# Kernel tuning notes

Measured on AMD Instinct MI355X. Metric: run time of the kernel, lower is better.

The kernel has to match this reference:

```python
import jax, jax.numpy as jnp
import numpy as np

B, L, D = 4096, 200, 64
N_ITEMS, N_USERS, N_RATINGS = 100000, 100000, 5


def setup_inputs() -> dict:
    key = jax.random.key(0)
    ks = jax.random.split(key, 10)
    nodes = jax.random.randint(ks[0], (B,), 0, N_USERS)
    history_uv = jax.random.randint(ks[1], (B, L), 0, N_ITEMS)
    history_r = jax.random.randint(ks[2], (B, L), 0, N_RATINGS)
    s = 1.0 / np.sqrt(D)
    v2e = jax.random.normal(ks[3], (N_ITEMS, D), dtype=jnp.float32)
    r2e = jax.random.normal(ks[4], (N_RATINGS, D), dtype=jnp.float32)
    # torch Linear: weight is [out, in]
    w1_W = jax.random.uniform(ks[5], (D, 2 * D), dtype=jnp.float32, minval=-s, maxval=s)
    w1_b = jax.random.uniform(ks[6], (D,), dtype=jnp.float32, minval=-s, maxval=s)
    w2_W = jax.random.uniform(ks[7], (D, D), dtype=jnp.float32, minval=-s, maxval=s)
    w2_b = jax.random.uniform(ks[8], (D,), dtype=jnp.float32, minval=-s, maxval=s)
    return {
        "v2e": v2e, "r2e": r2e,
        "w1_W": w1_W, "w1_b": w1_b, "w2_W": w2_W, "w2_b": w2_b,
        "nodes": nodes, "history_uv": history_uv, "history_r": history_r,
    }


def reference(v2e, r2e, w1_W, w1_b, w2_W, w2_b, nodes, history_uv, history_r):
    # Gather item and rating embeddings for every (node, history slot): [B, L, D]
    e_uv = v2e[history_uv]
    e_r = r2e[history_r]
    # concat -> [B, L, 2D], two-layer MLP with ReLU
    x = jnp.concatenate([e_uv, e_r], axis=-1)
    h = jax.nn.relu(jnp.einsum("bli,oi->blo", x, w1_W) + w1_b)
    o = jax.nn.relu(jnp.einsum("bli,oi->blo", h, w2_W) + w2_b)
    # uv=True branch: plain mean over the history dimension (nodes/u2e unused)
    return jnp.mean(o, axis=1)  # [B, D]
```

## Files before the change

### kernel.cpp

```cpp
#include <hip/hip_runtime.h>

#define NITEMS 100000
#define NRATE  5
#define BB     4096
#define LL     200
#define DD     64
#define NTILES 6250
#define NWAVES 2048

typedef short short8  __attribute__((ext_vector_type(8)));
typedef float f32x4   __attribute__((ext_vector_type(4)));
typedef float f32x2   __attribute__((ext_vector_type(2)));
typedef int   i32x4   __attribute__((ext_vector_type(4)));
typedef int   i32x2   __attribute__((ext_vector_type(2)));

static __device__ __forceinline__ short f2bf(float f) {
  return (short)((__builtin_bit_cast(unsigned, f) + 0x8000u) >> 16);
}
static __device__ __forceinline__ unsigned pk2bf(float a, float b) {
  const unsigned ua = __builtin_bit_cast(unsigned, a) + 0x8000u;
  const unsigned ub = __builtin_bit_cast(unsigned, b) + 0x8000u;
  return __builtin_amdgcn_perm(ub, ua, 0x07060302u);
}
static __device__ __forceinline__ int kperm(int p) {
  return ((p & 3) << 4) | (p >> 2);
}

__global__ __launch_bounds__(256) void k_pre(
    const float* __restrict__ v2e, const float* __restrict__ r2e,
    const float* __restrict__ w1W, const float* __restrict__ w1b,
    const float* __restrict__ w2W,
    unsigned char* __restrict__ pre8, short* __restrict__ w2p,
    float* __restrict__ r5p)
{
  const int tid = threadIdx.x;
  const int blk = blockIdx.x;

  if (blk >= 512) {
    for (int idx = tid; idx < 64 * 64; idx += 256) {
      const int o = idx >> 6, p = idx & 63;
      w2p[idx] = f2bf(w2W[o * 64 + kperm(p)]);
    }
    for (int idx = tid; idx < NRATE * 64; idx += 256) {
      const int r = idx >> 6, p = idx & 63;
      const int o = kperm(p);
      const float4* wr = reinterpret_cast<const float4*>(w1W + o * 128 + 64);
      const float4* rr = reinterpret_cast<const float4*>(r2e + r * 64);
      float s = w1b[o];
#pragma unroll
      for (int q = 0; q < 16; ++q) {
        const float4 a = wr[q], b = rr[q];
        s += a.x * b.x + a.y * b.y + a.z * b.z + a.w * b.w;
      }
      r5p[r * 64 + p] = s;
    }
    return;
  }

  const int wave = tid >> 6, lane = tid & 63;
  const int n = lane & 15, quad = lane >> 4;
  const int gw = blk * 4 + wave;
  const int ntile = (gw < (NTILES - 3 * NWAVES)) ? 4 : 3;

  const int q0 = ((n >> 1) & 3) * 16 + (n >> 3) * 8 + (n & 1) * 4;

  short8 bfr[2][4];
#pragma unroll
  for (int nt = 0; nt < 4; ++nt)
#pragma unroll
    for (int kh = 0; kh < 2; ++kh) {
      const float4* p = reinterpret_cast<const float4*>(
          w1W + (nt * 16 + n) * 128 + kh * 32 + quad * 8);
      const float4 x0 = p[0], x1 = p[1];
      i32x4 pk = {(int)pk2bf(x0.x, x0.y), (int)pk2bf(x0.z, x0.w),
                  (int)pk2bf(x1.x, x1.y), (int)pk2bf(x1.z, x1.w)};
      bfr[kh][nt] = __builtin_bit_cast(short8, pk);
    }

  int tile = gw;
  float4 cur0, cur1, cur2, cur3;
  {
    const size_t row = (size_t)(tile * 16 + n);
    const float4* p = reinterpret_cast<const float4*>(v2e + row * 64 + quad * 8);
    cur0 = p[0]; cur1 = p[1];
    const float4* q = reinterpret_cast<const float4*>(v2e + row * 64 + 32 + quad * 8);
    cur2 = q[0]; cur3 = q[1];
  }

  for (int it = 0; it < ntile; ++it) {
    const int next = tile + NWAVES;
    float4 nx0, nx1, nx2, nx3;
    if (it + 1 < ntile) {
      const size_t row = (size_t)(next * 16 + n);
      const float4* p = reinterpret_cast<const float4*>(v2e + row * 64 + quad * 8);
      nx0 = p[0]; nx1 = p[1];
      const float4* q = reinterpret_cast<const float4*>(v2e + row * 64 + 32 + quad * 8);
      nx2 = q[0]; nx3 = q[1];
    }

    short8 afr[2];
    {
      i32x4 pk0 = {(int)pk2bf(cur0.x, cur0.y), (int)pk2bf(cur0.z, cur0.w),
                   (int)pk2bf(cur1.x, cur1.y), (int)pk2bf(cur1.z, cur1.w)};
      afr[0] = __builtin_bit_cast(short8, pk0);
      i32x4 pk1 = {(int)pk2bf(cur2.x, cur2.y), (int)pk2bf(cur2.z, cur2.w),
                   (int)pk2bf(cur3.x, cur3.y), (int)pk2bf(cur3.z, cur3.w)};
      afr[1] = __builtin_bit_cast(short8, pk1);
    }

    f32x4 d[4];
#pragma unroll
    for (int nt = 0; nt < 4; ++nt) {
      f32x4 z = {0.f, 0.f, 0.f, 0.f};
      z = __builtin_amdgcn_mfma_f32_16x16x32_bf16(afr[0], bfr[0][nt], z, 0, 0, 0);
      z = __builtin_amdgcn_mfma_f32_16x16x32_bf16(afr[1], bfr[1][nt], z, 0, 0, 0);
      d[nt] = z;
    }

    const int ib = tile * 16;
#pragma unroll
    for (int r = 0; r < 4; ++r) {
      const int item = ib + quad * 4 + r;
      int pkd = 0;
      pkd = __builtin_amdgcn_cvt_pk_fp8_f32(d[0][r], d[1][r], pkd, false);
      pkd = __builtin_amdgcn_cvt_pk_fp8_f32(d[2][r], d[3][r], pkd, true);
      *reinterpret_cast<int*>(pre8 + (size_t)item * 64 + q0) = pkd;
    }

    tile = next;
    cur0 = nx0; cur1 = nx1; cur2 = nx2; cur3 = nx3;
  }
}

__global__ __launch_bounds__(256) void k_main(
    const unsigned char* __restrict__ pre8, const float* __restrict__ r5p,
    const short* __restrict__ w2p, const float* __restrict__ w2b,
    const int* __restrict__ huv, const int* __restrict__ hrr,
    float* __restrict__ out)
{
  __shared__ __align__(16) float s_r5[4][5 * 68];

  const int tid  = threadIdx.x;
  const int wave = tid >> 6, lane = tid & 63;
  const int n = lane & 15, quad = lane >> 4;
  const int b = blockIdx.x * 4 + wave;

#pragma unroll
  for (int i = 0; i < 5; ++i) {
    const int idx = i * 64 + lane;
    s_r5[wave][(idx >> 6) * 68 + (idx & 63)] = r5p[idx];
  }

  const int* hu = huv + b * LL;
  const int* hr = hrr + b * LL;

  int iv[13], ir[13];
#pragma unroll
  for (int t = 0; t < 12; ++t) {
    iv[t] = hu[t * 16 + n];
    ir[t] = hr[t * 16 + n];
  }
  {
    const int lc = min(192 + n, LL - 1);
    iv[12] = hu[lc];
    ir[12] = hr[lc];
  }

  i32x4 g[13];
#pragma unroll
  for (int t = 0; t < 13; ++t)
    g[t] = *reinterpret_cast<const i32x4*>(
        pre8 + (size_t)iv[t] * 64 + quad * 16);

  short8 bfr[2][4];
#pragma unroll
  for (int nt = 0; nt < 4; ++nt)
#pragma unroll
    for (int kh = 0; kh < 2; ++kh)
      bfr[kh][nt] = *reinterpret_cast<const short8*>(
          w2p + (nt * 16 + n) * 64 + kh * 32 + quad * 8);

  f32x4 zb[4];
#pragma unroll
  for (int nt = 0; nt < 4; ++nt) {
    const float bv = w2b[nt * 16 + n];
    zb[nt] = f32x4{bv, bv, bv, bv};
  }

  const float tailm = (quad < 2) ? 1.0f : 0.0f;
  f32x2 acc2[4] = {{0.f, 0.f}, {0.f, 0.f}, {0.f, 0.f}, {0.f, 0.f}};

#pragma unroll
  for (int t = 0; t < 13; ++t) {
    const float* rbase = &s_r5[wave][ir[t] * 68 + quad * 8];
    short8 afr[2];
    {
      const f32x2* rp = reinterpret_cast<const f32x2*>(rbase);
      f32x2 p0 = __builtin_amdgcn_cvt_pk_f32_fp8(g[t][0], false) + rp[0];
      f32x2 p1 = __builtin_amdgcn_cvt_pk_f32_fp8(g[t][0], true)  + rp[1];
      f32x2 p2 = __builtin_amdgcn_cvt_pk_f32_fp8(g[t][1], false) + rp[2];
      f32x2 p3 = __builtin_amdgcn_cvt_pk_f32_fp8(g[t][1], true)  + rp[3];
      i32x4 hpk = {
        (int)pk2bf(fmaxf(p0.x, 0.f), fmaxf(p0.y, 0.f)),
        (int)pk2bf(fmaxf(p1.x, 0.f), fmaxf(p1.y, 0.f)),
        (int)pk2bf(fmaxf(p2.x, 0.f), fmaxf(p2.y, 0.f)),
        (int)pk2bf(fmaxf(p3.x, 0.f), fmaxf(p3.y, 0.f))};
      afr[0] = __builtin_bit_cast(short8, hpk);
    }
    {
      const f32x2* rp = reinterpret_cast<const f32x2*>(rbase + 32);
      f32x2 p0 = __builtin_amdgcn_cvt_pk_f32_fp8(g[t][2], false) + rp[0];
      f32x2 p1 = __builtin_amdgcn_cvt_pk_f32_fp8(g[t][2], true)  + rp[1];
      f32x2 p2 = __builtin_amdgcn_cvt_pk_f32_fp8(g[t][3], false) + rp[2];
      f32x2 p3 = __builtin_amdgcn_cvt_pk_f32_fp8(g[t][3], true)  + rp[3];
      i32x4 hpk = {
        (int)pk2bf(fmaxf(p0.x, 0.f), fmaxf(p0.y, 0.f)),
        (int)pk2bf(fmaxf(p1.x, 0.f), fmaxf(p1.y, 0.f)),
        (int)pk2bf(fmaxf(p2.x, 0.f), fmaxf(p2.y, 0.f)),
        (int)pk2bf(fmaxf(p3.x, 0.f), fmaxf(p3.y, 0.f))};
      afr[1] = __builtin_bit_cast(short8, hpk);
    }

    f32x4 d[4];
#pragma unroll
    for (int nt = 0; nt < 4; ++nt) {
      f32x4 z = zb[nt];
      z = __builtin_amdgcn_mfma_f32_16x16x32_bf16(afr[0], bfr[0][nt], z, 0, 0, 0);
      z = __builtin_amdgcn_mfma_f32_16x16x32_bf16(afr[1], bfr[1][nt], z, 0, 0, 0);
      d[nt] = z;
    }

#pragma unroll
    for (int nt = 0; nt < 4; ++nt) {
      const float m0 = fmaxf(d[nt][0], 0.f), m1 = fmaxf(d[nt][1], 0.f);
      const float m2 = fmaxf(d[nt][2], 0.f), m3 = fmaxf(d[nt][3], 0.f);
      f32x2 s = {m0 + m1, m2 + m3};
      if (t == 12) { s.x *= tailm; s.y *= tailm; }
      acc2[nt] += s;
    }
  }

  float acc[4];
#pragma unroll
  for (int nt = 0; nt < 4; ++nt) {
    float v = acc2[nt].x + acc2[nt].y;
    v += __shfl_xor(v, 16, 64);
    v += __shfl_xor(v, 32, 64);
    acc[nt] = v;
  }

  out[b * 64 + quad * 16 + n] = acc[quad] * (1.0f / (float)LL);
}

__global__ __launch_bounds__(256) void k_fallback(
    const float* __restrict__ v2e, const float* __restrict__ r2e,
    const float* __restrict__ w1W, const float* __restrict__ w1b,
    const float* __restrict__ w2W, const float* __restrict__ w2b,
    const int* __restrict__ huv, const int* __restrict__ hrr,
    float* __restrict__ out)
{
  __shared__ float sw1[64][129];
  __shared__ float sw2[64][65];
  __shared__ float sx[4][128];
  __shared__ float sh[4][64];
  __shared__ float red[4][64];

  const int tid = threadIdx.x;
  const int wave = tid >> 6, lane = tid & 63;
  const int b = blockIdx.x;

  for (int idx = tid; idx < 64 * 128; idx += 256) sw1[idx >> 7][idx & 127] = w1W[idx];
  for (int idx = tid; idx < 64 * 64; idx += 256) sw2[idx >> 6][idx & 63] = w2W[idx];
  __syncthreads();

  const float b1o = w1b[lane], b2o = w2b[lane];
  float acc = 0.f;

  for (int l = wave; l < LL; l += 4) {
    const int iv = huv[b * LL + l];
    const int ir = hrr[b * LL + l];
    sx[wave][lane]      = v2e[iv * 64 + lane];
    sx[wave][64 + lane] = r2e[ir * 64 + lane];
    __syncthreads();
    float h = b1o;
    for (int i = 0; i < 128; ++i) h += sx[wave][i] * sw1[lane][i];
    sh[wave][lane] = fmaxf(h, 0.f);
    __syncthreads();
    float o = b2o;
    for (int i = 0; i < 64; ++i) o += sh[wave][i] * sw2[lane][i];
    acc += fmaxf(o, 0.f);
  }

  red[wave][lane] = acc;
  __syncthreads();
  if (tid < 64) {
    const float s = red[0][tid] + red[1][tid] + red[2][tid] + red[3][tid];
    out[b * 64 + tid] = s * (1.0f / (float)LL);
  }
}

extern "C" void kernel_launch(void* const* d_in, const int* in_sizes, int n_in,
                              void* d_out, int out_size, void* d_ws, size_t ws_size,
                              hipStream_t stream) {
  (void)in_sizes; (void)n_in; (void)out_size;
  const float* v2e = (const float*)d_in[0];
  const float* r2e = (const float*)d_in[1];
  const float* w1W = (const float*)d_in[2];
  const float* w1b = (const float*)d_in[3];
  const float* w2W = (const float*)d_in[4];
  const float* w2b = (const float*)d_in[5];
  const int* huv = (const int*)d_in[7];
  const int* hrr = (const int*)d_in[8];
  float* out = (float*)d_out;

  const size_t OFF_R5 = (size_t)NITEMS * 64;
  const size_t OFF_W2 = OFF_R5 + NRATE * 64 * sizeof(float);
  const size_t NEED   = OFF_W2 + 64 * 64 * sizeof(short);

  if (ws_size >= NEED) {
    unsigned char* pre8 = (unsigned char*)d_ws;
    float* r5p = (float*)((char*)d_ws + OFF_R5);
    short* w2p = (short*)((char*)d_ws + OFF_W2);

    k_pre<<<513, 256, 0, stream>>>(v2e, r2e, w1W, w1b, w2W, pre8, w2p, r5p);
    k_main<<<BB / 4, 256, 0, stream>>>(pre8, r5p, w2p, w2b, huv, hrr, out);
  } else {
    k_fallback<<<BB, 256, 0, stream>>>(v2e, r2e, w1W, w1b, w2W, w2b, huv, hrr, out);
  }
}
```

Baseline: 114.0 us.

## Split each batch row across two waves and flatten precompute to one tile per wave

k_pre now launches one wave per 16-item tile (1564 blocks) instead of a persistent loop with software prefetch, and moves the weight/rating precompute to block 0. k_main assigns two waves per batch row, each handling about half of the 13 history tiles, then combines the partial sums through shared memory with a block barrier. The aim is more parallelism and latency hiding for the gather-bound main kernel. In exchange it adds a __syncthreads and an LDS reduction, loads the same W2 fragments in twice as many waves, and raises launch overhead for the precompute. ReLU is also rewritten with vector max helpers.

```diff
diff --git a/kernel.cpp b/kernel.cpp
--- a/kernel.cpp
+++ b/kernel.cpp
@@ -6,13 +6,11 @@
 #define LL     200
 #define DD     64
 #define NTILES 6250
-#define NWAVES 2048
 
 typedef short short8  __attribute__((ext_vector_type(8)));
 typedef float f32x4   __attribute__((ext_vector_type(4)));
 typedef float f32x2   __attribute__((ext_vector_type(2)));
 typedef int   i32x4   __attribute__((ext_vector_type(4)));
-typedef int   i32x2   __attribute__((ext_vector_type(2)));
 
 static __device__ __forceinline__ short f2bf(float f) {
   return (short)((__builtin_bit_cast(unsigned, f) + 0x8000u) >> 16);
@@ -25,6 +23,22 @@
 static __device__ __forceinline__ int kperm(int p) {
   return ((p & 3) << 4) | (p >> 2);
 }
+
+#if __has_builtin(__builtin_elementwise_max)
+static __device__ __forceinline__ f32x2 relu2(f32x2 v) {
+  return __builtin_elementwise_max(v, f32x2{0.f, 0.f});
+}
+static __device__ __forceinline__ f32x4 relu4(f32x4 v) {
+  return __builtin_elementwise_max(v, f32x4{0.f, 0.f, 0.f, 0.f});
+}
+#else
+static __device__ __forceinline__ f32x2 relu2(f32x2 v) {
+  return f32x2{fmaxf(v.x, 0.f), fmaxf(v.y, 0.f)};
+}
+static __device__ __forceinline__ f32x4 relu4(f32x4 v) {
+  return f32x4{fmaxf(v[0], 0.f), fmaxf(v[1], 0.f), fmaxf(v[2], 0.f), fmaxf(v[3], 0.f)};
+}
+#endif
 
 __global__ __launch_bounds__(256) void k_pre(
     const float* __restrict__ v2e, const float* __restrict__ r2e,
@@ -36,7 +50,7 @@
   const int tid = threadIdx.x;
   const int blk = blockIdx.x;
 
-  if (blk >= 512) {
+  if (blk == 0) {
     for (int idx = tid; idx < 64 * 64; idx += 256) {
       const int o = idx >> 6, p = idx & 63;
       w2p[idx] = f2bf(w2W[o * 64 + kperm(p)]);
@@ -59,10 +73,15 @@
 
   const int wave = tid >> 6, lane = tid & 63;
   const int n = lane & 15, quad = lane >> 4;
-  const int gw = blk * 4 + wave;
-  const int ntile = (gw < (NTILES - 3 * NWAVES)) ? 4 : 3;
+  const int tile = (blk - 1) * 4 + wave;
+  if (tile >= NTILES) return;
 
   const int q0 = ((n >> 1) & 3) * 16 + (n >> 3) * 8 + (n & 1) * 4;
+
+  const size_t row = (size_t)(tile * 16 + n);
+  const float4* pv = reinterpret_cast<const float4*>(v2e + row * 64 + quad * 8);
+  const float4* qv = reinterpret_cast<const float4*>(v2e + row * 64 + 32 + quad * 8);
+  const float4 cur0 = pv[0], cur1 = pv[1], cur2 = qv[0], cur3 = qv[1];
 
   short8 bfr[2][4];
 #pragma unroll
@@ -77,58 +96,100 @@
       bfr[kh][nt] = __builtin_bit_cast(short8, pk);
     }
 
-  int tile = gw;
-  float4 cur0, cur1, cur2, cur3;
+  short8 afr[2];
   {
-    const size_t row = (size_t)(tile * 16 + n);
-    const float4* p = reinterpret_cast<const float4*>(v2e + row * 64 + quad * 8);
-    cur0 = p[0]; cur1 = p[1];
-    const float4* q = reinterpret_cast<const float4*>(v2e + row * 64 + 32 + quad * 8);
-    cur2 = q[0]; cur3 = q[1];
-  }
-
-  for (int it = 0; it < ntile; ++it) {
-    const int next = tile + NWAVES;
-    float4 nx0, nx1, nx2, nx3;
-    if (it + 1 < ntile) {
-      const size_t row = (size_t)(next * 16 + n);
-      const float4* p = reinterpret_cast<const float4*>(v2e + row * 64 + quad * 8);
-      nx0 = p[0]; nx1 = p[1];
-      const float4* q = reinterpret_cast<const float4*>(v2e + row * 64 + 32 + quad * 8);
-      nx2 = q[0]; nx3 = q[1];
-    }
-
+    i32x4 pk0 = {(int)pk2bf(cur0.x, cur0.y), (int)pk2bf(cur0.z, cur0.w),
+                 (int)pk2bf(cur1.x, cur1.y), (int)pk2bf(cur1.z, cur1.w)};
+    afr[0] = __builtin_bit_cast(short8, pk0);
+    i32x4 pk1 = {(int)pk2bf(cur2.x, cur2.y), (int)pk2bf(cur2.z, cur2.w),
+                 (int)pk2bf(cur3.x, cur3.y), (int)pk2bf(cur3.z, cur3.w)};
+    afr[1] = __builtin_bit_cast(short8, pk1);
+  }
+
+  f32x4 d[4];
+#pragma unroll
+  for (int nt = 0; nt < 4; ++nt) {
+    f32x4 z = {0.f, 0.f, 0.f, 0.f};
+    z = __builtin_amdgcn_mfma_f32_16x16x32_bf16(afr[0], bfr[0][nt], z, 0, 0, 0);
+    z = __builtin_amdgcn_mfma_f32_16x16x32_bf16(afr[1], bfr[1][nt], z, 0, 0, 0);
+    d[nt] = z;
+  }
+
+  const int ib = tile * 16;
+#pragma unroll
+  for (int r = 0; r < 4; ++r) {
+    const int item = ib + quad * 4 + r;
+    int pkd = 0;
+    pkd = __builtin_amdgcn_cvt_pk_fp8_f32(d[0][r], d[1][r], pkd, false);
+    pkd = __builtin_amdgcn_cvt_pk_fp8_f32(d[2][r], d[3][r], pkd, true);
+    *reinterpret_cast<int*>(pre8 + (size_t)item * 64 + q0) = pkd;
+  }
+}
+
+template<int T0, int NT>
+static __device__ __forceinline__ void mbody(
+    const unsigned char* __restrict__ pre8,
+    const int* __restrict__ hu, const int* __restrict__ hr,
+    const float* __restrict__ r5w,
+    const short8 (&bfr)[2][4], const f32x4 (&zb)[4],
+    const int n, const int quad, const float tailm,
+    f32x4 (&acc4)[4])
+{
+  int ivv[NT], irr[NT];
+#pragma unroll
+  for (int k = 0; k < NT; ++k) {
+    const int t = T0 + k;
+    const int l = (t == 12) ? min(192 + n, LL - 1) : (t * 16 + n);
+    ivv[k] = hu[l];
+    irr[k] = hr[l];
+  }
+
+  i32x4 g[NT];
+#pragma unroll
+  for (int k = 0; k < NT; ++k)
+    g[k] = *reinterpret_cast<const i32x4*>(
+        pre8 + (size_t)ivv[k] * 64 + quad * 16);
+
+#pragma unroll
+  for (int k = 0; k < NT; ++k) {
+    const float* rbase = r5w + irr[k] * 68 + quad * 8;
     short8 afr[2];
     {
-      i32x4 pk0 = {(int)pk2bf(cur0.x, cur0.y), (int)pk2bf(cur0.z, cur0.w),
-                   (int)pk2bf(cur1.x, cur1.y), (int)pk2bf(cur1.z, cur1.w)};
-      afr[0] = __builtin_bit_cast(short8, pk0);
-      i32x4 pk1 = {(int)pk2bf(cur2.x, cur2.y), (int)pk2bf(cur2.z, cur2.w),
-                   (int)pk2bf(cur3.x, cur3.y), (int)pk2bf(cur3.z, cur3.w)};
-      afr[1] = __builtin_bit_cast(short8, pk1);
+      const f32x2* rp = reinterpret_cast<const f32x2*>(rbase);
+      f32x2 p0 = relu2(__builtin_amdgcn_cvt_pk_f32_fp8(g[k][0], false) + rp[0]);
+      f32x2 p1 = relu2(__builtin_amdgcn_cvt_pk_f32_fp8(g[k][0], true)  + rp[1]);
+      f32x2 p2 = relu2(__builtin_amdgcn_cvt_pk_f32_fp8(g[k][1], false) + rp[2]);
+      f32x2 p3 = relu2(__builtin_amdgcn_cvt_pk_f32_fp8(g[k][1], true)  + rp[3]);
+      i32x4 hpk = {(int)pk2bf(p0.x, p0.y), (int)pk2bf(p1.x, p1.y),
+                   (int)pk2bf(p2.x, p2.y), (int)pk2bf(p3.x, p3.y)};
+      afr[0] = __builtin_bit_cast(short8, hpk);
+    }
+    {
+      const f32x2* rp = reinterpret_cast<const f32x2*>(rbase + 32);
+      f32x2 p0 = relu2(__builtin_amdgcn_cvt_pk_f32_fp8(g[k][2], false) + rp[0]);
+      f32x2 p1 = relu2(__builtin_amdgcn_cvt_pk_f32_fp8(g[k][2], true)  + rp[1]);
+      f32x2 p2 = relu2(__builtin_amdgcn_cvt_pk_f32_fp8(g[k][3], false) + rp[2]);
+      f32x2 p3 = relu2(__builtin_amdgcn_cvt_pk_f32_fp8(g[k][3], true)  + rp[3]);
+      i32x4 hpk = {(int)pk2bf(p0.x, p0.y), (int)pk2bf(p1.x, p1.y),
+                   (int)pk2bf(p2.x, p2.y), (int)pk2bf(p3.x, p3.y)};
+      afr[1] = __builtin_bit_cast(short8, hpk);
     }
 
     f32x4 d[4];
 #pragma unroll
     for (int nt = 0; nt < 4; ++nt) {
-      f32x4 z = {0.f, 0.f, 0.f, 0.f};
+      f32x4 z = zb[nt];
       z = __builtin_amdgcn_mfma_f32_16x16x32_bf16(afr[0], bfr[0][nt], z, 0, 0, 0);
       z = __builtin_amdgcn_mfma_f32_16x16x32_bf16(afr[1], bfr[1][nt], z, 0, 0, 0);
       d[nt] = z;
     }
 
-    const int ib = tile * 16;
-#pragma unroll
-    for (int r = 0; r < 4; ++r) {
-      const int item = ib + quad * 4 + r;
-      int pkd = 0;
-      pkd = __builtin_amdgcn_cvt_pk_fp8_f32(d[0][r], d[1][r], pkd, false);
-      pkd = __builtin_amdgcn_cvt_pk_fp8_f32(d[2][r], d[3][r], pkd, true);
-      *reinterpret_cast<int*>(pre8 + (size_t)item * 64 + q0) = pkd;
-    }
-
-    tile = next;
-    cur0 = nx0; cur1 = nx1; cur2 = nx2; cur3 = nx3;
+#pragma unroll
+    for (int nt = 0; nt < 4; ++nt) {
+      f32x4 mx = relu4(d[nt]);
+      if (T0 + k == 12) mx = mx * tailm;
+      acc4[nt] += mx;
+    }
   }
 }
 
@@ -139,11 +200,13 @@
     float* __restrict__ out)
 {
   __shared__ __align__(16) float s_r5[4][5 * 68];
+  __shared__ float red[4][64];
 
   const int tid  = threadIdx.x;
   const int wave = tid >> 6, lane = tid & 63;
   const int n = lane & 15, quad = lane >> 4;
-  const int b = blockIdx.x * 4 + wave;
+  const int hlf = wave & 1;
+  const int b = blockIdx.x * 2 + (wave >> 1);
 
 #pragma unroll
   for (int i = 0; i < 5; ++i) {
@@ -154,24 +217,6 @@
   const int* hu = huv + b * LL;
   const int* hr = hrr + b * LL;
 
-  int iv[13], ir[13];
-#pragma unroll
-  for (int t = 0; t < 12; ++t) {
-    iv[t] = hu[t * 16 + n];
-    ir[t] = hr[t * 16 + n];
-  }
-  {
-    const int lc = min(192 + n, LL - 1);
-    iv[12] = hu[lc];
-    ir[12] = hr[lc];
-  }
-
-  i32x4 g[13];
-#pragma unroll
-  for (int t = 0; t < 13; ++t)
-    g[t] = *reinterpret_cast<const i32x4*>(
-        pre8 + (size_t)iv[t] * 64 + quad * 16);
-
   short8 bfr[2][4];
 #pragma unroll
   for (int nt = 0; nt < 4; ++nt)
@@ -188,68 +233,30 @@
   }
 
   const float tailm = (quad < 2) ? 1.0f : 0.0f;
-  f32x2 acc2[4] = {{0.f, 0.f}, {0.f, 0.f}, {0.f, 0.f}, {0.f, 0.f}};
-
-#pragma unroll
-  for (int t = 0; t < 13; ++t) {
-    const float* rbase = &s_r5[wave][ir[t] * 68 + quad * 8];
-    short8 afr[2];
-    {
-      const f32x2* rp = reinterpret_cast<const f32x2*>(rbase);
-      f32x2 p0 = __builtin_amdgcn_cvt_pk_f32_fp8(g[t][0], false) + rp[0];
-      f32x2 p1 = __builtin_amdgcn_cvt_pk_f32_fp8(g[t][0], true)  + rp[1];
-      f32x2 p2 = __builtin_amdgcn_cvt_pk_f32_fp8(g[t][1], false) + rp[2];
-      f32x2 p3 = __builtin_amdgcn_cvt_pk_f32_fp8(g[t][1], true)  + rp[3];
-      i32x4 hpk = {
-        (int)pk2bf(fmaxf(p0.x, 0.f), fmaxf(p0.y, 0.f)),
-        (int)pk2bf(fmaxf(p1.x, 0.f), fmaxf(p1.y, 0.f)),
-        (int)pk2bf(fmaxf(p2.x, 0.f), fmaxf(p2.y, 0.f)),
-        (int)pk2bf(fmaxf(p3.x, 0.f), fmaxf(p3.y, 0.f))};
-      afr[0] = __builtin_bit_cast(short8, hpk);
-    }
-    {
-      const f32x2* rp = reinterpret_cast<const f32x2*>(rbase + 32);
-      f32x2 p0 = __builtin_amdgcn_cvt_pk_f32_fp8(g[t][2], false) + rp[0];
-      f32x2 p1 = __builtin_amdgcn_cvt_pk_f32_fp8(g[t][2], true)  + rp[1];
-      f32x2 p2 = __builtin_amdgcn_cvt_pk_f32_fp8(g[t][3], false) + rp[2];
-      f32x2 p3 = __builtin_amdgcn_cvt_pk_f32_fp8(g[t][3], true)  + rp[3];
-      i32x4 hpk = {
-        (int)pk2bf(fmaxf(p0.x, 0.f), fmaxf(p0.y, 0.f)),
-        (int)pk2bf(fmaxf(p1.x, 0.f), fmaxf(p1.y, 0.f)),
-        (int)pk2bf(fmaxf(p2.x, 0.f), fmaxf(p2.y, 0.f)),
-        (int)pk2bf(fmaxf(p3.x, 0.f), fmaxf(p3.y, 0.f))};
-      afr[1] = __builtin_bit_cast(short8, hpk);
-    }
-
-    f32x4 d[4];
-#pragma unroll
-    for (int nt = 0; nt < 4; ++nt) {
-      f32x4 z = zb[nt];
-      z = __builtin_amdgcn_mfma_f32_16x16x32_bf16(afr[0], bfr[0][nt], z, 0, 0, 0);
-      z = __builtin_amdgcn_mfma_f32_16x16x32_bf16(afr[1], bfr[1][nt], z, 0, 0, 0);
-      d[nt] = z;
-    }
-
-#pragma unroll
-    for (int nt = 0; nt < 4; ++nt) {
-      const float m0 = fmaxf(d[nt][0], 0.f), m1 = fmaxf(d[nt][1], 0.f);
-      const float m2 = fmaxf(d[nt][2], 0.f), m3 = fmaxf(d[nt][3], 0.f);
-      f32x2 s = {m0 + m1, m2 + m3};
-      if (t == 12) { s.x *= tailm; s.y *= tailm; }
-      acc2[nt] += s;
-    }
-  }
+  f32x4 acc4[4] = {{0.f,0.f,0.f,0.f},{0.f,0.f,0.f,0.f},
+                   {0.f,0.f,0.f,0.f},{0.f,0.f,0.f,0.f}};
+
+  if (hlf == 0)
+    mbody<0, 7>(pre8, hu, hr, &s_r5[wave][0], bfr, zb, n, quad, tailm, acc4);
+  else
+    mbody<7, 6>(pre8, hu, hr, &s_r5[wave][0], bfr, zb, n, quad, tailm, acc4);
 
   float acc[4];
 #pragma unroll
   for (int nt = 0; nt < 4; ++nt) {
-    float v = acc2[nt].x + acc2[nt].y;
+    float v = (acc4[nt][0] + acc4[nt][1]) + (acc4[nt][2] + acc4[nt][3]);
     v += __shfl_xor(v, 16, 64);
     v += __shfl_xor(v, 32, 64);
     acc[nt] = v;
   }
 
-  out[b * 64 + quad * 16 + n] = acc[quad] * (1.0f / (float)LL);
+  red[wave][quad * 16 + n] = acc[quad];
+  __syncthreads();
+  if (wave < 2) {
+    const int bb = blockIdx.x * 2 + wave;
+    out[bb * 64 + lane] =
+        (red[2 * wave][lane] + red[2 * wave + 1][lane]) * (1.0f / (float)LL);
+  }
 }
 
 __global__ __launch_bounds__(256) void k_fallback(
@@ -322,8 +329,8 @@
     float* r5p = (float*)((char*)d_ws + OFF_R5);
     short* w2p = (short*)((char*)d_ws + OFF_W2);
 
-    k_pre<<<513, 256, 0, stream>>>(v2e, r2e, w1W, w1b, w2W, pre8, w2p, r5p);
-    k_main<<<BB / 4, 256, 0, stream>>>(pre8, r5p, w2p, w2b, huv, hrr, out);
+    k_pre<<<1564, 256, 0, stream>>>(v2e, r2e, w1W, w1b, w2W, pre8, w2p, r5p);
+    k_main<<<BB / 2, 256, 0, stream>>>(pre8, r5p, w2p, w2b, huv, hrr, out);
   } else {
     k_fallback<<<BB, 256, 0, stream>>>(v2e, r2e, w1W, w1b, w2W, w2b, huv, hrr, out);
   }
```

Result: slower. 119.6 us (+5.0%).
